# Kernel tuning notes

Hardware: AMD Instinct MI355X
Metric: run time of the kernel (lower is better)

## Reference

```python
import jax, jax.numpy as jnp
import numpy as np

B, D, S, O = 32768, 1024, 64, 4  # batch, feature_dim, n_subjects, n_outputs


def setup_inputs() -> dict:
    key = jax.random.key(0)
    kx, ks, kw, kb = jax.random.split(key, 4)
    x = jax.random.normal(kx, (B, D), dtype=jnp.float32)          # backbone features
    subject_ids = jax.random.randint(ks, (B,), 0, S)              # per-sample head id
    W = jax.random.normal(kw, (S, D, O), dtype=jnp.float32) / np.float32(np.sqrt(D))
    b = jax.random.normal(kb, (S, O), dtype=jnp.float32) * 0.01
    return {"x": x, "subject_ids": subject_ids, "W": W, "b": b}


def reference(x, subject_ids, W, b):
    # Vectorized form of the per-subject loop:
    #   for sid in unique(subject_ids): outputs[idxs] = heads[sid](features[idxs])
    # Each head is Linear(D, O): out[i] = x[i] @ W[sid[i]] + b[sid[i]].
    Wg = jnp.take(W, subject_ids, axis=0)   # [B, D, O] gathered per-sample weights
    bg = jnp.take(b, subject_ids, axis=0)   # [B, O]
    return jnp.einsum('bd,bdo->bo', x, Wg) + bg
```

## Files before the change

### kernel.cpp

```cpp
#include <hip/hip_runtime.h>

constexpr int B = 32768;
constexpr int D = 1024;
constexpr int S = 64;
constexpr int O = 4;

constexpr int BLOCKS_PER_SID = 16;
constexpr int MAIN_BLOCKS    = S * BLOCKS_PER_SID;
constexpr int WAVES_PER_SID  = BLOCKS_PER_SID * 4;

#define WS_OFFSETS 0
#define WS_PERM    256

__global__ __launch_bounds__(1024) void sort_kernel(const int* __restrict__ sid,
                                                    int* __restrict__ ws) {
    __shared__ int h[S];
    __shared__ int off[S];
    const int t = threadIdx.x;
    if (t < S) h[t] = 0;
    __syncthreads();

    int myR[B / 1024];
    int myS[B / 1024];
    #pragma unroll
    for (int it = 0; it < B / 1024; ++it) {
        const int i = it * 1024 + t;
        const int s = sid[i];
        myS[it] = s;
        myR[it] = atomicAdd(&h[s], 1);
    }
    __syncthreads();

    if (t == 0) {
        int acc = 0;
        for (int s2 = 0; s2 < S; ++s2) {
            off[s2] = acc;
            ws[WS_OFFSETS + s2] = acc;
            acc += h[s2];
        }
        ws[WS_OFFSETS + S] = acc;
    }
    __syncthreads();

    #pragma unroll
    for (int it = 0; it < B / 1024; ++it) {
        const int i = it * 1024 + t;
        ws[WS_PERM + off[myS[it]] + myR[it]] = i;
    }
}

__global__ __launch_bounds__(256) void main_kernel(const float* __restrict__ x,
                                                   const float* __restrict__ W,
                                                   const float* __restrict__ bias,
                                                   const int* __restrict__ ws,
                                                   float* __restrict__ out) {
    __shared__ float4 Wl[D];

    const int s    = blockIdx.x / BLOCKS_PER_SID;
    const int blk  = blockIdx.x % BLOCKS_PER_SID;
    const int wave = threadIdx.x >> 6;
    const int lane = threadIdx.x & 63;

    const float4* __restrict__ Wg = (const float4*)(W + (size_t)s * (D * O));
    for (int d = threadIdx.x; d < D; d += 256) Wl[d] = Wg[d];
    __syncthreads();

    float4 w[4][4];
    #pragma unroll
    for (int k = 0; k < 4; ++k)
        #pragma unroll
        for (int j = 0; j < 4; ++j)
            w[k][j] = Wl[k * 256 + lane * 4 + j];

    const int start = ws[WS_OFFSETS + s];
    const int cnt   = ws[WS_OFFSETS + s + 1] - start;
    const int wv_id = blk * 4 + wave;

    const int   q  = (lane >> 2) & 3;
    const float bb = bias[s * O + q];

    int i   = wv_id;
    int row = (i < cnt) ? ws[WS_PERM + start + i] : 0;
    while (i < cnt) {
        const int i_next   = i + WAVES_PER_SID;
        const int row_next = (i_next < cnt) ? ws[WS_PERM + start + i_next] : 0;

        const float* __restrict__ xr = x + (size_t)row * D;
        float a0 = 0.f, a1 = 0.f, a2 = 0.f, a3 = 0.f;
        #pragma unroll
        for (int k = 0; k < 4; ++k) {
            const float4 xv = *(const float4*)(xr + k * 256 + lane * 4);
            a0 += xv.x * w[k][0].x + xv.y * w[k][1].x + xv.z * w[k][2].x + xv.w * w[k][3].x;
            a1 += xv.x * w[k][0].y + xv.y * w[k][1].y + xv.z * w[k][2].y + xv.w * w[k][3].y;
            a2 += xv.x * w[k][0].z + xv.y * w[k][1].z + xv.z * w[k][2].z + xv.w * w[k][3].z;
            a3 += xv.x * w[k][0].w + xv.y * w[k][1].w + xv.z * w[k][2].w + xv.w * w[k][3].w;
        }

        #pragma unroll
        for (int m = 4; m <= 32; m <<= 1) {
            a0 += __shfl_xor(a0, m, 64);
            a1 += __shfl_xor(a1, m, 64);
            a2 += __shfl_xor(a2, m, 64);
            a3 += __shfl_xor(a3, m, 64);
        }
        float v = (q == 0) ? a0 : (q == 1) ? a1 : (q == 2) ? a2 : a3;
        v += __shfl_xor(v, 1, 64);
        v += __shfl_xor(v, 2, 64);

        if (lane < 16 && (lane & 3) == 0)
            out[(size_t)row * O + q] = v + bb;

        i   = i_next;
        row = row_next;
    }
}

extern "C" void kernel_launch(void* const* d_in, const int* in_sizes, int n_in,
                              void* d_out, int out_size, void* d_ws, size_t ws_size,
                              hipStream_t stream) {
    const float* x    = (const float*)d_in[0];
    const int*   sid  = (const int*)d_in[1];
    const float* W    = (const float*)d_in[2];
    const float* bias = (const float*)d_in[3];
    float* out = (float*)d_out;
    int* ws = (int*)d_ws;

    sort_kernel<<<1, 1024, 0, stream>>>(sid, ws);
    main_kernel<<<MAIN_BLOCKS, 256, 0, stream>>>(x, W, bias, ws, out);
}
```

Baseline: 222.6 us.

## Parallelize counting sort into histogram, scan, and scatter kernels

Replaces the single-block counting sort of subject ids with a three-kernel multi-block sort: per-block histograms over 64 blocks, a single-wave scan that computes global offsets and per-block bases, and a per-block scatter. The intent is to spread the serial sort's single-workgroup latency across many CUs. In exchange it adds two extra kernel launches and more global-memory round trips for the histograms.

```diff
diff --git a/kernel.cpp b/kernel.cpp
--- a/kernel.cpp
+++ b/kernel.cpp
@@ -9,44 +9,68 @@
 constexpr int MAIN_BLOCKS    = S * BLOCKS_PER_SID;
 constexpr int WAVES_PER_SID  = BLOCKS_PER_SID * 4;
 
+constexpr int SORT_BLOCKS   = 64;
+constexpr int ROWS_PER_SBLK = B / SORT_BLOCKS;
+
 #define WS_OFFSETS 0
-#define WS_PERM    256
+#define WS_BASE    128
+#define WS_HIST    8192
+#define WS_PERM    16384
 
-__global__ __launch_bounds__(1024) void sort_kernel(const int* __restrict__ sid,
-                                                    int* __restrict__ ws) {
+__global__ __launch_bounds__(256) void hist_kernel(const int* __restrict__ sid,
+                                                   int* __restrict__ ws) {
     __shared__ int h[S];
-    __shared__ int off[S];
-    const int t = threadIdx.x;
+    const int t = threadIdx.x, b = blockIdx.x;
     if (t < S) h[t] = 0;
     __syncthreads();
+    const int rbase = b * ROWS_PER_SBLK;
+    atomicAdd(&h[sid[rbase + t]], 1);
+    atomicAdd(&h[sid[rbase + 256 + t]], 1);
+    __syncthreads();
+    if (t < S) ws[WS_HIST + b * S + t] = h[t];
+}
 
-    int myR[B / 1024];
-    int myS[B / 1024];
+__global__ __launch_bounds__(64) void scan_kernel(int* __restrict__ ws) {
+    __shared__ int tot[S];
+    __shared__ int off[S + 1];
+    const int s = threadIdx.x;
+    int basev[SORT_BLOCKS];
+    int acc = 0;
     #pragma unroll
-    for (int it = 0; it < B / 1024; ++it) {
-        const int i = it * 1024 + t;
-        const int s = sid[i];
-        myS[it] = s;
-        myR[it] = atomicAdd(&h[s], 1);
+    for (int b = 0; b < SORT_BLOCKS; ++b) {
+        basev[b] = acc;
+        acc += ws[WS_HIST + b * S + s];
+    }
+    tot[s] = acc;
+    __syncthreads();
+    if (s == 0) {
+        int a = 0;
+        for (int i = 0; i < S; ++i) { off[i] = a; a += tot[i]; }
+        off[S] = a;
     }
     __syncthreads();
+    const int o = off[s];
+    ws[WS_OFFSETS + s] = o;
+    if (s == 0) ws[WS_OFFSETS + S] = off[S];
+    #pragma unroll
+    for (int b = 0; b < SORT_BLOCKS; ++b)
+        ws[WS_BASE + b * S + s] = basev[b] + o;
+}
 
-    if (t == 0) {
-        int acc = 0;
-        for (int s2 = 0; s2 < S; ++s2) {
-            off[s2] = acc;
-            ws[WS_OFFSETS + s2] = acc;
-            acc += h[s2];
-        }
-        ws[WS_OFFSETS + S] = acc;
-    }
+__global__ __launch_bounds__(256) void scatter_kernel(const int* __restrict__ sid,
+                                                      int* __restrict__ ws) {
+    __shared__ int cur[S];
+    __shared__ int bas[S];
+    const int t = threadIdx.x, b = blockIdx.x;
+    if (t < S) { cur[t] = 0; bas[t] = ws[WS_BASE + b * S + t]; }
     __syncthreads();
-
-    #pragma unroll
-    for (int it = 0; it < B / 1024; ++it) {
-        const int i = it * 1024 + t;
-        ws[WS_PERM + off[myS[it]] + myR[it]] = i;
-    }
+    const int rbase = b * ROWS_PER_SBLK;
+    const int i0 = rbase + t, i1 = rbase + 256 + t;
+    const int s0 = sid[i0], s1 = sid[i1];
+    const int r0 = atomicAdd(&cur[s0], 1);
+    const int r1 = atomicAdd(&cur[s1], 1);
+    ws[WS_PERM + bas[s0] + r0] = i0;
+    ws[WS_PERM + bas[s1] + r1] = i1;
 }
 
 __global__ __launch_bounds__(256) void main_kernel(const float* __restrict__ x,
@@ -125,6 +149,8 @@
     float* out = (float*)d_out;
     int* ws = (int*)d_ws;
 
-    sort_kernel<<<1, 1024, 0, stream>>>(sid, ws);
-    main_kernel<<<MAIN_BLOCKS, 256, 0, stream>>>(x, W, bias, ws, out);
+    hist_kernel   <<<SORT_BLOCKS, 256, 0, stream>>>(sid, ws);
+    scan_kernel   <<<1,            64, 0, stream>>>(ws);
+    scatter_kernel<<<SORT_BLOCKS, 256, 0, stream>>>(sid, ws);
+    main_kernel   <<<MAIN_BLOCKS, 256, 0, stream>>>(x, W, bias, ws, out);
 }
```

New measurement: 205.9 us. 7.5% less time.
